# Optimization experiments

Measured on AMD Instinct MI355X. Metric: run time of the kernel, lower is better.

## Reference

```python
import jax, jax.numpy as jnp
import numpy as np

D_MODEL = 1024
N_HEADS = 16
B, T = 2, 2048


def setup_inputs() -> dict:
    key = jax.random.key(0)
    ks = jax.random.split(key, 5)
    scale = 1.0 / np.sqrt(D_MODEL)
    return {
        "x": jax.random.normal(ks[0], (B, T, D_MODEL), dtype=jnp.float32),
        "W_q": jax.random.normal(ks[1], (D_MODEL, D_MODEL), dtype=jnp.float32) * scale,
        "W_k": jax.random.normal(ks[2], (D_MODEL, D_MODEL), dtype=jnp.float32) * scale,
        "W_v": jax.random.normal(ks[3], (D_MODEL, D_MODEL), dtype=jnp.float32) * scale,
        "W_o": jax.random.normal(ks[4], (D_MODEL, D_MODEL), dtype=jnp.float32) * scale,
    }


def reference(x, W_q, W_k, W_v, W_o):
    Bn, Tn, D = x.shape
    H = N_HEADS
    Dh = D // H
    # nn.Linear(x) = x @ W.T ; weights stored as [out, in]
    q = (x @ W_q.T).reshape(Bn, Tn, H, Dh).transpose(0, 2, 1, 3)  # [B,H,T,Dh]
    k = (x @ W_k.T).reshape(Bn, Tn, H, Dh).transpose(0, 2, 1, 3)
    v = (x @ W_v.T).reshape(Bn, Tn, H, Dh).transpose(0, 2, 1, 3)
    scores = jnp.einsum("bhqd,bhkd->bhqk", q, k) / np.sqrt(Dh).astype(np.float32)
    attn = jax.nn.softmax(scores, axis=-1)  # [B,H,T,T]
    out = jnp.einsum("bhqk,bhkd->bhqd", attn, v)  # [B,H,T,Dh]
    out = out.transpose(0, 2, 1, 3).reshape(Bn, Tn, D)
    return out @ W_o.T
```

## Files before the change

### kernel.cpp

```cpp
#include <hip/hip_runtime.h>
#include <stdint.h>
#include <stddef.h>


typedef __bf16  bf16x8  __attribute__((ext_vector_type(8)));
typedef __bf16  bf16x4  __attribute__((ext_vector_type(4)));
typedef float   floatx4 __attribute__((ext_vector_type(4)));

#define DEV static __device__ __forceinline__

DEV void ld_g2l16(const void* g, void* l) {
    __builtin_amdgcn_global_load_lds(
        (__attribute__((address_space(1))) void*)g,
        (__attribute__((address_space(3))) void*)l,
        16, 0, 0);
}

#define WK_SCALE 0.18033688011112042f

__global__ __launch_bounds__(256) void cvt_all(
    const float* __restrict__ x,
    const float* __restrict__ wq, const float* __restrict__ wk,
    const float* __restrict__ wv, const float* __restrict__ wo,
    __bf16* __restrict__ xb,
    __bf16* __restrict__ wqb, __bf16* __restrict__ wkb,
    __bf16* __restrict__ wvb, __bf16* __restrict__ wob)
{
    unsigned u = blockIdx.x * 256u + threadIdx.x;
    const float* src;
    __bf16* dst;
    unsigned off;
    float mul = 1.0f;
    if (u < 1048576u) {
        src = x; dst = xb; off = u;
    } else {
        unsigned u2 = u - 1048576u;
        unsigned sel = u2 >> 18;
        off = u2 & 0x3FFFFu;
        src = (sel == 0) ? wq : (sel == 1) ? wk : (sel == 2) ? wv : wo;
        dst = (sel == 0) ? wqb : (sel == 1) ? wkb : (sel == 2) ? wvb : wob;
        if (sel == 1) mul = WK_SCALE;
    }
    float4 f = *(const float4*)(src + (size_t)off * 4);
    bf16x4 o = { (__bf16)(f.x * mul), (__bf16)(f.y * mul),
                 (__bf16)(f.z * mul), (__bf16)(f.w * mul) };
    *(bf16x4*)(dst + (size_t)off * 4) = o;
}

template<int NMAT, bool OUT_F32>
__global__ __launch_bounds__(256) void gemm_bt(
    const __bf16* __restrict__ A,
    const __bf16* __restrict__ B0, const __bf16* __restrict__ B1,
    const __bf16* __restrict__ B2,
    void* __restrict__ C0, void* __restrict__ C1, void* __restrict__ C2)
{
    constexpr int Kd = 1024;
    constexpr int N  = 1024;
    __shared__ __bf16 As[128 * 32];
    __shared__ __bf16 Bs[128 * 32];

    const int t    = threadIdx.x;
    const int wid  = __builtin_amdgcn_readfirstlane(t >> 6);
    const int lane = t & 63;
    const int quad = lane >> 4;
    const int l15  = lane & 15;

    const int bx  = blockIdx.x;
    const int mat = (NMAT > 1) ? (bx >> 3) : 0;
    const int bn  = (NMAT > 1) ? (bx & 7)  : bx;
    const int bm  = blockIdx.y;
    const __bf16* Bm = (mat == 0) ? B0 : (mat == 1) ? B1 : B2;

    const __bf16* pA[2];
    const __bf16* pB[2];
#pragma unroll
    for (int i = 0; i < 2; ++i) {
        int c    = i * 256 + t;
        int row  = c >> 2;
        int g    = (c & 3) ^ ((row >> 1) & 3);
        pA[i] = A  + (size_t)(bm * 128 + row) * Kd + g * 8;
        pB[i] = Bm + (size_t)(bn * 128 + row) * Kd + g * 8;
    }

    const int wm = wid >> 1;
    const int wn = wid & 1;
    const int slotr = quad ^ ((l15 >> 1) & 3);

    floatx4 acc[4][4];
    const floatx4 z = { 0.f, 0.f, 0.f, 0.f };
#pragma unroll
    for (int i = 0; i < 4; ++i)
#pragma unroll
        for (int j = 0; j < 4; ++j) acc[i][j] = z;

    for (int kb = 0; kb < Kd; kb += 32) {
        __syncthreads();
#pragma unroll
        for (int i = 0; i < 2; ++i) {
            ld_g2l16(pA[i] + kb, (char*)As + i * 4096 + wid * 1024);
            ld_g2l16(pB[i] + kb, (char*)Bs + i * 4096 + wid * 1024);
        }
        __syncthreads();

        bf16x8 af[4], bf[4];
#pragma unroll
        for (int i = 0; i < 4; ++i) {
            int rowA = wm * 64 + i * 16 + l15;
            af[i] = *(const bf16x8*)&As[rowA * 32 + slotr * 8];
            int rowB = wn * 64 + i * 16 + l15;
            bf[i] = *(const bf16x8*)&Bs[rowB * 32 + slotr * 8];
        }
#pragma unroll
        for (int i = 0; i < 4; ++i)
#pragma unroll
            for (int j = 0; j < 4; ++j)
                acc[i][j] = __builtin_amdgcn_mfma_f32_16x16x32_bf16(
                    af[i], bf[j], acc[i][j], 0, 0, 0);
    }

    void* Cv = (mat == 0) ? C0 : (mat == 1) ? C1 : C2;
    const int row0 = bm * 128 + wm * 64;
    const int col0 = bn * 128 + wn * 64;
#pragma unroll
    for (int i = 0; i < 4; ++i)
#pragma unroll
        for (int j = 0; j < 4; ++j)
#pragma unroll
            for (int r = 0; r < 4; ++r) {
                int grow = row0 + i * 16 + quad * 4 + r;
                int gcol = col0 + j * 16 + l15;
                if (OUT_F32)
                    ((float*)Cv)[(size_t)grow * N + gcol] = acc[i][j][r];
                else
                    ((__bf16*)Cv)[(size_t)grow * N + gcol] = (__bf16)acc[i][j][r];
            }
}

__global__ __launch_bounds__(256) void transpose_v(
    const __bf16* __restrict__ V, __bf16* __restrict__ Vt)
{
    __shared__ __bf16 tile[64 * 72];
    const int t  = threadIdx.x;
    const int kt = blockIdx.x;
    const int bh = blockIdx.y;
    const int b  = bh >> 4, h = bh & 15;

#pragma unroll
    for (int rr = 0; rr < 64; rr += 32) {
        int row = rr + (t >> 3), ch = t & 7;
        uint4 v = *(const uint4*)(V + (size_t)(b * 2048 + kt * 64 + row) * 1024
                                    + h * 64 + ch * 8);
        *(uint4*)&tile[row * 72 + ch * 8] = v;
    }
    __syncthreads();
#pragma unroll
    for (int dd = 0; dd < 64; dd += 32) {
        int d = dd + (t >> 3), ch = t & 7;
        bf16x8 val;
#pragma unroll
        for (int j = 0; j < 8; ++j) val[j] = tile[(ch * 8 + j) * 72 + d];
        *(bf16x8*)(Vt + (size_t)(bh * 64 + d) * 2048 + kt * 64 + ch * 8) = val;
    }
}

__global__ __launch_bounds__(256, 2) void flash_kernel(
    const __bf16* __restrict__ Q, const __bf16* __restrict__ K,
    const __bf16* __restrict__ Vt, __bf16* __restrict__ O)
{
    __shared__ __bf16 Qs[128 * 64];
    __shared__ __bf16 Ks[2][64 * 64];
    __shared__ __bf16 Vs[2][64 * 64];
    __shared__ __bf16 Ps[4][32 * 72];

    const int t    = threadIdx.x;
    const int wid  = __builtin_amdgcn_readfirstlane(t >> 6);
    const int lane = t & 63;
    const int quad = lane >> 4;
    const int l15  = lane & 15;
    const int qt   = blockIdx.x;
    const int bh   = blockIdx.y;
    const int b    = bh >> 4, h = bh & 15;

#pragma unroll
    for (int i = 0; i < 4; ++i) {
        int c = i * 256 + t;
        int row = c >> 3;
        int g   = (c & 7) ^ (row & 7);
        ld_g2l16(Q + (size_t)(b * 2048 + qt * 128 + row) * 1024 + h * 64 + g * 8,
                 (char*)Qs + i * 4096 + wid * 1024);
    }
#define ISSUE_KV(KT, BUF)                                                      \
    do {                                                                       \
        _Pragma("unroll")                                                      \
        for (int i_ = 0; i_ < 2; ++i_) {                                       \
            int c_ = i_ * 256 + t;                                             \
            int row_ = c_ >> 3;                                                \
            int g_   = (c_ & 7) ^ (row_ & 7);                                  \
            ld_g2l16(K + (size_t)(b * 2048 + (KT) * 64 + row_) * 1024          \
                         + h * 64 + g_ * 8,                                    \
                     (char*)Ks[BUF] + i_ * 4096 + wid * 1024);                 \
            ld_g2l16(Vt + (size_t)(bh * 64 + row_) * 2048 + (KT) * 64 + g_ * 8,\
                     (char*)Vs[BUF] + i_ * 4096 + wid * 1024);                 \
        }                                                                      \
    } while (0)

    ISSUE_KV(0, 0);
    __syncthreads();

    bf16x8 qf[2][2];
#pragma unroll
    for (int nb = 0; nb < 2; ++nb)
#pragma unroll
        for (int ks = 0; ks < 2; ++ks) {
            int row  = wid * 32 + nb * 16 + l15;
            int slot = (ks * 4 + quad) ^ (row & 7);
            qf[nb][ks] = *(const bf16x8*)&Qs[row * 64 + slot * 8];
        }

    const floatx4 z = { 0.f, 0.f, 0.f, 0.f };
    floatx4 o[2][4];
#pragma unroll
    for (int mq = 0; mq < 2; ++mq)
#pragma unroll
        for (int nd = 0; nd < 4; ++nd) o[mq][nd] = z;
    float lsum[2] = { 0.f, 0.f };

    for (int kt = 0; kt < 32; ++kt) {
        const int cur = kt & 1;
        if (kt) __syncthreads();
        if (kt < 31) ISSUE_KV(kt + 1, cur ^ 1);

        floatx4 s[4][2];
#pragma unroll
        for (int mk = 0; mk < 4; ++mk)
#pragma unroll
            for (int nb = 0; nb < 2; ++nb) s[mk][nb] = z;
#pragma unroll
        for (int ks = 0; ks < 2; ++ks)
#pragma unroll
            for (int mk = 0; mk < 4; ++mk) {
                int rowk = mk * 16 + l15;
                int slot = (ks * 4 + quad) ^ (rowk & 7);
                bf16x8 kf = *(const bf16x8*)&Ks[cur][rowk * 64 + slot * 8];
#pragma unroll
                for (int nb = 0; nb < 2; ++nb)
                    s[mk][nb] = __builtin_amdgcn_mfma_f32_16x16x32_bf16(
                        kf, qf[nb][ks], s[mk][nb], 0, 0, 0);
            }

#pragma unroll
        for (int mk = 0; mk < 4; ++mk)
#pragma unroll
            for (int nb = 0; nb < 2; ++nb) {
                float p0 = __builtin_amdgcn_exp2f(s[mk][nb][0]);
                float p1 = __builtin_amdgcn_exp2f(s[mk][nb][1]);
                float p2 = __builtin_amdgcn_exp2f(s[mk][nb][2]);
                float p3 = __builtin_amdgcn_exp2f(s[mk][nb][3]);
                lsum[nb] += (p0 + p1) + (p2 + p3);
                bf16x4 pw = { (__bf16)p0, (__bf16)p1, (__bf16)p2, (__bf16)p3 };
                *(bf16x4*)&Ps[wid][(nb * 16 + l15) * 72 + mk * 16 + quad * 4] = pw;
            }
        asm volatile("s_waitcnt lgkmcnt(0)" ::: "memory");

#pragma unroll
        for (int ks = 0; ks < 2; ++ks) {
            bf16x8 pa[2];
#pragma unroll
            for (int mq = 0; mq < 2; ++mq)
                pa[mq] = *(const bf16x8*)
                    &Ps[wid][(mq * 16 + l15) * 72 + (ks * 4 + quad) * 8];
#pragma unroll
            for (int nd = 0; nd < 4; ++nd) {
                int rowd = nd * 16 + l15;
                int slot = (ks * 4 + quad) ^ (rowd & 7);
                bf16x8 vf = *(const bf16x8*)&Vs[cur][rowd * 64 + slot * 8];
#pragma unroll
                for (int mq = 0; mq < 2; ++mq)
                    o[mq][nd] = __builtin_amdgcn_mfma_f32_16x16x32_bf16(
                        pa[mq], vf, o[mq][nd], 0, 0, 0);
            }
        }
    }
#undef ISSUE_KV

#pragma unroll
    for (int nb = 0; nb < 2; ++nb) {
        lsum[nb] += __shfl_xor(lsum[nb], 16);
        lsum[nb] += __shfl_xor(lsum[nb], 32);
    }
#pragma unroll
    for (int mq = 0; mq < 2; ++mq)
#pragma unroll
        for (int reg = 0; reg < 4; ++reg) {
            float lv  = __shfl(lsum[mq], quad * 4 + reg);
            float inv = 1.f / lv;
            int trow = qt * 128 + wid * 32 + mq * 16 + quad * 4 + reg;
#pragma unroll
            for (int nd = 0; nd < 4; ++nd)
                O[(size_t)(b * 2048 + trow) * 1024 + h * 64 + nd * 16 + l15] =
                    (__bf16)(o[mq][nd][reg] * inv);
        }
}

extern "C" void kernel_launch(void* const* d_in, const int* in_sizes, int n_in,
                              void* d_out, int out_size, void* d_ws, size_t ws_size,
                              hipStream_t stream)
{
    const float* x  = (const float*)d_in[0];
    const float* wq = (const float*)d_in[1];
    const float* wk = (const float*)d_in[2];
    const float* wv = (const float*)d_in[3];
    const float* wo = (const float*)d_in[4];

    char* ws = (char*)d_ws;
    __bf16* xb  = (__bf16*)(ws + 0);
    __bf16* wqb = (__bf16*)(ws + 8388608);
    __bf16* wkb = (__bf16*)(ws + 10485760);
    __bf16* wvb = (__bf16*)(ws + 12582912);
    __bf16* wob = (__bf16*)(ws + 14680064);
    __bf16* Qb  = (__bf16*)(ws + 16777216);
    __bf16* Kb  = (__bf16*)(ws + 25165824);
    __bf16* Vb  = (__bf16*)(ws + 33554432);
    __bf16* Vtb = (__bf16*)(ws + 41943040);
    __bf16* Ob  = xb;

    cvt_all<<<8192, 256, 0, stream>>>(x, wq, wk, wv, wo, xb, wqb, wkb, wvb, wob);

    gemm_bt<3, false><<<dim3(24, 32), 256, 0, stream>>>(
        xb, wqb, wkb, wvb, (void*)Qb, (void*)Kb, (void*)Vb);

    transpose_v<<<dim3(32, 32), 256, 0, stream>>>(Vb, Vtb);

    flash_kernel<<<dim3(16, 32), 256, 0, stream>>>(Qb, Kb, Vtb, Ob);

    gemm_bt<1, true><<<dim3(8, 32), 256, 0, stream>>>(
        Ob, wob, nullptr, nullptr, d_out, nullptr, nullptr);
}
```

Baseline: 196.9 us.

## Keep P in registers for PV via 16x16x16 MFMA, shrink output GEMM tile

The flash kernel no longer stages softmax probabilities through shared memory. It computes S one 16-key slice at a time, with K as the A operand so the result is S transposed, and feeds the bf16 P fragments straight into 16x16x16 MFMAs against V^T read from LDS. This removes the P LDS write, the waitcnt and the P reload, and frees LDS so occupancy can go to 3 blocks per CU. The output projection GEMM now uses a 64-row M tile to launch twice as many blocks, and the O store is vectorized to bf16x4. The cost is twice as many smaller MFMA instructions in the PV step and more register pressure.

```diff
diff --git a/kernel.cpp b/kernel.cpp
--- a/kernel.cpp
+++ b/kernel.cpp
@@ -6,6 +6,7 @@
 typedef __bf16  bf16x8  __attribute__((ext_vector_type(8)));
 typedef __bf16  bf16x4  __attribute__((ext_vector_type(4)));
 typedef float   floatx4 __attribute__((ext_vector_type(4)));
+typedef short   short4v __attribute__((ext_vector_type(4)));
 
 #define DEV static __device__ __forceinline__
 
@@ -14,6 +15,17 @@
         (__attribute__((address_space(1))) void*)g,
         (__attribute__((address_space(3))) void*)l,
         16, 0, 0);
+}
+
+DEV floatx4 mfma16(bf16x4 a, bf16x4 b, floatx4 c) {
+#if defined(__HIP_DEVICE_COMPILE__)
+    return __builtin_amdgcn_mfma_f32_16x16x16bf16_1k(
+        __builtin_bit_cast(short4v, a), __builtin_bit_cast(short4v, b),
+        c, 0, 0, 0);
+#else
+    (void)a; (void)b;
+    return c;
+#endif
 }
 
 #define WK_SCALE 0.18033688011112042f
@@ -47,7 +59,7 @@
     *(bf16x4*)(dst + (size_t)off * 4) = o;
 }
 
-template<int NMAT, bool OUT_F32>
+template<int BM, int NMAT, bool OUT_F32>
 __global__ __launch_bounds__(256) void gemm_bt(
     const __bf16* __restrict__ A,
     const __bf16* __restrict__ B0, const __bf16* __restrict__ B1,
@@ -56,7 +68,9 @@
 {
     constexpr int Kd = 1024;
     constexpr int N  = 1024;
-    __shared__ __bf16 As[128 * 32];
+    constexpr int MI = BM / 32;
+    constexpr int NA = BM / 64;
+    __shared__ __bf16 As[BM * 32];
     __shared__ __bf16 Bs[128 * 32];
 
     const int t    = threadIdx.x;
@@ -71,14 +85,20 @@
     const int bm  = blockIdx.y;
     const __bf16* Bm = (mat == 0) ? B0 : (mat == 1) ? B1 : B2;
 
-    const __bf16* pA[2];
+    const __bf16* pA[NA];
     const __bf16* pB[2];
+#pragma unroll
+    for (int i = 0; i < NA; ++i) {
+        int c    = i * 256 + t;
+        int row  = c >> 2;
+        int g    = (c & 3) ^ ((row >> 1) & 3);
+        pA[i] = A + (size_t)(bm * BM + row) * Kd + g * 8;
+    }
 #pragma unroll
     for (int i = 0; i < 2; ++i) {
         int c    = i * 256 + t;
         int row  = c >> 2;
         int g    = (c & 3) ^ ((row >> 1) & 3);
-        pA[i] = A  + (size_t)(bm * 128 + row) * Kd + g * 8;
         pB[i] = Bm + (size_t)(bn * 128 + row) * Kd + g * 8;
     }
 
@@ -86,32 +106,36 @@
     const int wn = wid & 1;
     const int slotr = quad ^ ((l15 >> 1) & 3);
 
-    floatx4 acc[4][4];
+    floatx4 acc[MI][4];
     const floatx4 z = { 0.f, 0.f, 0.f, 0.f };
 #pragma unroll
-    for (int i = 0; i < 4; ++i)
+    for (int i = 0; i < MI; ++i)
 #pragma unroll
         for (int j = 0; j < 4; ++j) acc[i][j] = z;
 
     for (int kb = 0; kb < Kd; kb += 32) {
         __syncthreads();
 #pragma unroll
-        for (int i = 0; i < 2; ++i) {
+        for (int i = 0; i < NA; ++i)
             ld_g2l16(pA[i] + kb, (char*)As + i * 4096 + wid * 1024);
+#pragma unroll
+        for (int i = 0; i < 2; ++i)
             ld_g2l16(pB[i] + kb, (char*)Bs + i * 4096 + wid * 1024);
-        }
         __syncthreads();
 
-        bf16x8 af[4], bf[4];
-#pragma unroll
-        for (int i = 0; i < 4; ++i) {
-            int rowA = wm * 64 + i * 16 + l15;
+        bf16x8 af[MI], bf[4];
+#pragma unroll
+        for (int i = 0; i < MI; ++i) {
+            int rowA = wm * (BM / 2) + i * 16 + l15;
             af[i] = *(const bf16x8*)&As[rowA * 32 + slotr * 8];
-            int rowB = wn * 64 + i * 16 + l15;
-            bf[i] = *(const bf16x8*)&Bs[rowB * 32 + slotr * 8];
-        }
-#pragma unroll
-        for (int i = 0; i < 4; ++i)
+        }
+#pragma unroll
+        for (int j = 0; j < 4; ++j) {
+            int rowB = wn * 64 + j * 16 + l15;
+            bf[j] = *(const bf16x8*)&Bs[rowB * 32 + slotr * 8];
+        }
+#pragma unroll
+        for (int i = 0; i < MI; ++i)
 #pragma unroll
             for (int j = 0; j < 4; ++j)
                 acc[i][j] = __builtin_amdgcn_mfma_f32_16x16x32_bf16(
@@ -119,10 +143,10 @@
     }
 
     void* Cv = (mat == 0) ? C0 : (mat == 1) ? C1 : C2;
-    const int row0 = bm * 128 + wm * 64;
+    const int row0 = bm * BM + wm * (BM / 2);
     const int col0 = bn * 128 + wn * 64;
 #pragma unroll
-    for (int i = 0; i < 4; ++i)
+    for (int i = 0; i < MI; ++i)
 #pragma unroll
         for (int j = 0; j < 4; ++j)
 #pragma unroll
@@ -163,14 +187,13 @@
     }
 }
 
-__global__ __launch_bounds__(256, 2) void flash_kernel(
+__global__ __launch_bounds__(256, 3) void flash_kernel(
     const __bf16* __restrict__ Q, const __bf16* __restrict__ K,
     const __bf16* __restrict__ Vt, __bf16* __restrict__ O)
 {
     __shared__ __bf16 Qs[128 * 64];
     __shared__ __bf16 Ks[2][64 * 64];
     __shared__ __bf16 Vs[2][64 * 64];
-    __shared__ __bf16 Ps[4][32 * 72];
 
     const int t    = threadIdx.x;
     const int wid  = __builtin_amdgcn_readfirstlane(t >> 6);
@@ -220,9 +243,9 @@
     const floatx4 z = { 0.f, 0.f, 0.f, 0.f };
     floatx4 o[2][4];
 #pragma unroll
-    for (int mq = 0; mq < 2; ++mq)
-#pragma unroll
-        for (int nd = 0; nd < 4; ++nd) o[mq][nd] = z;
+    for (int nb = 0; nb < 2; ++nb)
+#pragma unroll
+        for (int nd = 0; nd < 4; ++nd) o[nb][nd] = z;
     float lsum[2] = { 0.f, 0.f };
 
     for (int kt = 0; kt < 32; ++kt) {
@@ -230,54 +253,40 @@
         if (kt) __syncthreads();
         if (kt < 31) ISSUE_KV(kt + 1, cur ^ 1);
 
-        floatx4 s[4][2];
-#pragma unroll
-        for (int mk = 0; mk < 4; ++mk)
-#pragma unroll
-            for (int nb = 0; nb < 2; ++nb) s[mk][nb] = z;
-#pragma unroll
-        for (int ks = 0; ks < 2; ++ks)
-#pragma unroll
-            for (int mk = 0; mk < 4; ++mk) {
-                int rowk = mk * 16 + l15;
+#pragma unroll
+        for (int kt16 = 0; kt16 < 4; ++kt16) {
+            floatx4 s[2] = { z, z };
+#pragma unroll
+            for (int ks = 0; ks < 2; ++ks) {
+                int rowk = kt16 * 16 + l15;
                 int slot = (ks * 4 + quad) ^ (rowk & 7);
                 bf16x8 kf = *(const bf16x8*)&Ks[cur][rowk * 64 + slot * 8];
 #pragma unroll
                 for (int nb = 0; nb < 2; ++nb)
-                    s[mk][nb] = __builtin_amdgcn_mfma_f32_16x16x32_bf16(
-                        kf, qf[nb][ks], s[mk][nb], 0, 0, 0);
+                    s[nb] = __builtin_amdgcn_mfma_f32_16x16x32_bf16(
+                        kf, qf[nb][ks], s[nb], 0, 0, 0);
             }
-
-#pragma unroll
-        for (int mk = 0; mk < 4; ++mk)
+            bf16x4 pb[2];
 #pragma unroll
             for (int nb = 0; nb < 2; ++nb) {
-                float p0 = __builtin_amdgcn_exp2f(s[mk][nb][0]);
-                float p1 = __builtin_amdgcn_exp2f(s[mk][nb][1]);
-                float p2 = __builtin_amdgcn_exp2f(s[mk][nb][2]);
-                float p3 = __builtin_amdgcn_exp2f(s[mk][nb][3]);
+                float p0 = __builtin_amdgcn_exp2f(s[nb][0]);
+                float p1 = __builtin_amdgcn_exp2f(s[nb][1]);
+                float p2 = __builtin_amdgcn_exp2f(s[nb][2]);
+                float p3 = __builtin_amdgcn_exp2f(s[nb][3]);
                 lsum[nb] += (p0 + p1) + (p2 + p3);
                 bf16x4 pw = { (__bf16)p0, (__bf16)p1, (__bf16)p2, (__bf16)p3 };
-                *(bf16x4*)&Ps[wid][(nb * 16 + l15) * 72 + mk * 16 + quad * 4] = pw;
+                pb[nb] = pw;
             }
-        asm volatile("s_waitcnt lgkmcnt(0)" ::: "memory");
-
-#pragma unroll
-        for (int ks = 0; ks < 2; ++ks) {
-            bf16x8 pa[2];
-#pragma unroll
-            for (int mq = 0; mq < 2; ++mq)
-                pa[mq] = *(const bf16x8*)
-                    &Ps[wid][(mq * 16 + l15) * 72 + (ks * 4 + quad) * 8];
 #pragma unroll
             for (int nd = 0; nd < 4; ++nd) {
-                int rowd = nd * 16 + l15;
-                int slot = (ks * 4 + quad) ^ (rowd & 7);
-                bf16x8 vf = *(const bf16x8*)&Vs[cur][rowd * 64 + slot * 8];
-#pragma unroll
-                for (int mq = 0; mq < 2; ++mq)
-                    o[mq][nd] = __builtin_amdgcn_mfma_f32_16x16x32_bf16(
-                        pa[mq], vf, o[mq][nd], 0, 0, 0);
+                int row  = nd * 16 + l15;
+                int g    = kt16 * 2 + (quad >> 1);
+                int slot = g ^ (row & 7);
+                bf16x4 va = *(const bf16x4*)
+                    &Vs[cur][row * 64 + slot * 8 + (quad & 1) * 4];
+#pragma unroll
+                for (int nb = 0; nb < 2; ++nb)
+                    o[nb][nd] = mfma16(va, pb[nb], o[nb][nd]);
             }
         }
     }
@@ -289,17 +298,19 @@
         lsum[nb] += __shfl_xor(lsum[nb], 32);
     }
 #pragma unroll
-    for (int mq = 0; mq < 2; ++mq)
-#pragma unroll
-        for (int reg = 0; reg < 4; ++reg) {
-            float lv  = __shfl(lsum[mq], quad * 4 + reg);
-            float inv = 1.f / lv;
-            int trow = qt * 128 + wid * 32 + mq * 16 + quad * 4 + reg;
-#pragma unroll
-            for (int nd = 0; nd < 4; ++nd)
-                O[(size_t)(b * 2048 + trow) * 1024 + h * 64 + nd * 16 + l15] =
-                    (__bf16)(o[mq][nd][reg] * inv);
-        }
+    for (int nb = 0; nb < 2; ++nb) {
+        float inv = 1.f / lsum[nb];
+        int token = qt * 128 + wid * 32 + nb * 16 + l15;
+#pragma unroll
+        for (int nd = 0; nd < 4; ++nd) {
+            bf16x4 ov = { (__bf16)(o[nb][nd][0] * inv),
+                          (__bf16)(o[nb][nd][1] * inv),
+                          (__bf16)(o[nb][nd][2] * inv),
+                          (__bf16)(o[nb][nd][3] * inv) };
+            *(bf16x4*)(O + (size_t)(b * 2048 + token) * 1024
+                         + h * 64 + nd * 16 + quad * 4) = ov;
+        }
+    }
 }
 
 extern "C" void kernel_launch(void* const* d_in, const int* in_sizes, int n_in,
@@ -326,13 +337,13 @@
 
     cvt_all<<<8192, 256, 0, stream>>>(x, wq, wk, wv, wo, xb, wqb, wkb, wvb, wob);
 
-    gemm_bt<3, false><<<dim3(24, 32), 256, 0, stream>>>(
+    gemm_bt<128, 3, false><<<dim3(24, 32), 256, 0, stream>>>(
         xb, wqb, wkb, wvb, (void*)Qb, (void*)Kb, (void*)Vb);
 
     transpose_v<<<dim3(32, 32), 256, 0, stream>>>(Vb, Vtb);
 
     flash_kernel<<<dim3(16, 32), 256, 0, stream>>>(Qb, Kb, Vtb, Ob);
 
-    gemm_bt<1, true><<<dim3(8, 32), 256, 0, stream>>>(
+    gemm_bt<64, 1, true><<<dim3(8, 64), 256, 0, stream>>>(
         Ob, wob, nullptr, nullptr, d_out, nullptr, nullptr);
 }
```

After: 188.9 us. 4.0% less time.
